# Kernel optimization log

Measured on AMD Instinct MI355X. Metric: run time of the kernel, lower is better.

Reference implementation:

```python
import jax, jax.numpy as jnp
import numpy as np

N = 131072   # batch
D = 32       # num features (main subnets)
P = 32       # num interaction pairs
H_MAIN = 64  # hidden_dim_main
H_INTER = 64 # hidden_dim_inter


def setup_inputs() -> dict:
    key = jax.random.key(0)
    ks = jax.random.split(key, 7)
    X = jax.random.normal(ks[0], (N, D), dtype=jnp.float32)
    # cyclic interaction pairs (i, (i+1) % D), matching init_kwargs literal
    pairs = jnp.asarray(np.stack([np.arange(P), (np.arange(P) + 1) % D], axis=1), dtype=jnp.int32)
    # stacked ExU params for the D main subnets: log_weight [H,1] -> [D,H], bias [1] -> [D]
    log_w_main = (jax.random.normal(ks[1], (D, H_MAIN), dtype=jnp.float32) * 0.1)
    bias_main = jnp.zeros((D,), dtype=jnp.float32)
    v_main = jax.random.normal(ks[2], (D, H_MAIN), dtype=jnp.float32) / np.float32(np.sqrt(H_MAIN))
    # stacked ExU params for the P interaction subnets: log_weight [H,2], bias [2]
    log_w_inter = (jax.random.normal(ks[3], (P, H_INTER, 2), dtype=jnp.float32) * 0.1)
    bias_inter = jnp.zeros((P, 2), dtype=jnp.float32)
    v_inter = jax.random.normal(ks[4], (P, H_INTER), dtype=jnp.float32) / np.float32(np.sqrt(H_INTER))
    # final Linear(D+P, 1)
    W_final = jax.random.normal(ks[5], (D + P,), dtype=jnp.float32) / np.float32(np.sqrt(D + P))
    b_final = jnp.zeros((), dtype=jnp.float32)
    return {
        "X": X,
        "log_w_main": log_w_main,
        "bias_main": bias_main,
        "v_main": v_main,
        "log_w_inter": log_w_inter,
        "bias_inter": bias_inter,
        "v_inter": v_inter,
        "W_final": W_final,
        "b_final": b_final,
        "pairs": pairs,
    }


def reference(X, log_w_main, bias_main, v_main, log_w_inter, bias_inter, v_inter, W_final, b_final, pairs):
    # Main subnets, batched over features: ExU(1,H) is (x - b) * exp(log_w)
    h_main = jax.nn.silu((X - bias_main[None, :])[:, :, None] * jnp.exp(log_w_main)[None, :, :])  # [N,D,H]
    m_out = jnp.einsum('ndh,dh->nd', h_main, v_main)  # [N,D]
    # Interaction subnets, batched over pairs: gather the 2 columns per pair
    Xp = X[:, pairs]  # [N,P,2]
    h_int = jax.nn.silu(jnp.einsum('npc,phc->nph', Xp - bias_inter[None, :, :], jnp.exp(log_w_inter)))  # [N,P,H]
    i_out = jnp.einsum('nph,ph->np', h_int, v_inter)  # [N,P]
    Z = jnp.concatenate([m_out, i_out], axis=1)  # [N, D+P]
    out = Z @ W_final + b_final  # [N]
    return out, Z
```

## Files before the change

kernel.cpp:

```cpp
#include <hip/hip_runtime.h>

#define DD 32
#define PP 32
#define HH 64
#define TPB 512
#define ROWS 512

#define M_NE 128
#define M_LO (-8.0f)
#define M_HI (8.0f)
#define I_NE 96
#define I_LO (-6.5f)
#define I_HI (6.5f)
#define I_CELLS (I_NE * I_NE)

#define BTPB 256
#define MAIN_BLOCKS ((DD * M_NE) / BTPB)
#define BLOCKS_PER_P (I_CELLS / BTPB)
#define INTER_BLOCKS (PP * BLOCKS_PER_P)

#define TSTR 36
#define XSTR 33

__device__ __forceinline__ float silu_fast(float t) {
    const float LOG2E = 1.4426950408889634f;
    return t * __builtin_amdgcn_rcpf(1.f + __builtin_amdgcn_exp2f(-t * LOG2E));
}

__device__ __forceinline__ unsigned short f2bf(float f) {
    unsigned u = __float_as_uint(f);
    u += 0x7FFF + ((u >> 16) & 1);
    return (unsigned short)(u >> 16);
}

__device__ __forceinline__ float bf2f(unsigned short s) {
    return __uint_as_float((unsigned)s << 16);
}

__global__ void build_luts(const float* __restrict__ lwm,
                           const float* __restrict__ vm,
                           const float* __restrict__ lwi,
                           const float* __restrict__ vi,
                           float* __restrict__ LUTm,
                           unsigned short* __restrict__ LUTi)
{
    const float LOG2E = 1.4426950408889634f;
    __shared__ float2 sew[HH];
    __shared__ float  sv[HH];

    if (blockIdx.x < MAIN_BLOCKS) {
        const float h = (M_HI - M_LO) / (float)(M_NE - 1);
        int idx = blockIdx.x * BTPB + threadIdx.x;
        int d = idx >> 7;
        int i = idx & (M_NE - 1);
        float s = M_LO + (float)i * h;
        float acc = 0.f;
        #pragma unroll 8
        for (int k = 0; k < HH; ++k) {
            float w = __builtin_amdgcn_exp2f(lwm[d * HH + k] * LOG2E);
            acc = fmaf(silu_fast(s * w), vm[d * HH + k], acc);
        }
        LUTm[idx] = acc;
    } else {
        const float h = (I_HI - I_LO) / (float)(I_NE - 1);
        const int rel = blockIdx.x - MAIN_BLOCKS;
        const int p   = rel / BLOCKS_PER_P;
        const int cip = (rel % BLOCKS_PER_P) * BTPB + threadIdx.x;
        const int i   = cip / I_NE;
        const int j   = cip - i * I_NE;
        if (threadIdx.x < HH) {
            int t = threadIdx.x;
            sew[t] = make_float2(
                __builtin_amdgcn_exp2f(lwi[(p * HH + t) * 2 + 0] * LOG2E),
                __builtin_amdgcn_exp2f(lwi[(p * HH + t) * 2 + 1] * LOG2E));
            sv[t] = vi[p * HH + t];
        }
        __syncthreads();
        float c0 = I_LO + (float)i * h;
        float c1 = I_LO + (float)j * h;
        float acc = 0.f;
        #pragma unroll 8
        for (int k = 0; k < HH; ++k) {
            float a = fmaf(c0, sew[k].x, c1 * sew[k].y);
            acc = fmaf(silu_fast(a), sv[k], acc);
        }
        unsigned short ab = f2bf(acc);
        unsigned short* cb = LUTi + (size_t)p * I_CELLS * 4;
        if (i < I_NE - 1 && j < I_NE - 1) cb[((i    ) * I_NE + j    ) * 4 + 0] = ab;
        if (i < I_NE - 1 && j > 0)        cb[((i    ) * I_NE + j - 1) * 4 + 1] = ab;
        if (i > 0        && j < I_NE - 1) cb[((i - 1) * I_NE + j    ) * 4 + 2] = ab;
        if (i > 0        && j > 0)        cb[((i - 1) * I_NE + j - 1) * 4 + 3] = ab;
    }
}

__global__ __launch_bounds__(TPB, 2) void qgam_main(
    const float* __restrict__ X,
    const float* __restrict__ bias_main,
    const float* __restrict__ bias_inter,
    const float* __restrict__ W_final,
    const float* __restrict__ b_final,
    const int* __restrict__ pairs,
    const float* __restrict__ LUTm,
    const ushort4* __restrict__ LUTi,
    float* __restrict__ out,
    float* __restrict__ Zout,
    int nrows)
{
    const float M_INVH = (float)(M_NE - 1) / (M_HI - M_LO);
    const float I_INVH = (float)(I_NE - 1) / (I_HI - I_LO);

    __shared__ float s_lutm[DD * M_NE];
    __shared__ float s_x[ROWS][XSTR];
    __shared__ float s_t[ROWS][TSTR];
    __shared__ float s_wf[DD + PP];
    __shared__ float s_moff[DD];
    __shared__ float s_io0[PP], s_io1[PP];
    __shared__ int   s_p0[PP], s_p1[PP];

    const int tid  = threadIdx.x;
    const int base = blockIdx.x * ROWS;

    {
        const float4* __restrict__ lm4 = reinterpret_cast<const float4*>(LUTm);
        float4* __restrict__ sl4 = reinterpret_cast<float4*>(s_lutm);
        #pragma unroll
        for (int k = 0; k < 2; ++k)
            sl4[k * TPB + tid] = lm4[k * TPB + tid];
    }
    {
        const float4* __restrict__ Xv =
            reinterpret_cast<const float4*>(X) + (size_t)base * (DD / 4);
        #pragma unroll
        for (int k = 0; k < 8; ++k) {
            const int fi = k * TPB + tid;
            const int rl = fi >> 3;
            const int c  = (fi & 7) * 4;
            if (base + rl < nrows) {
                float4 v = Xv[fi];
                s_x[rl][c + 0] = v.x;
                s_x[rl][c + 1] = v.y;
                s_x[rl][c + 2] = v.z;
                s_x[rl][c + 3] = v.w;
            }
        }
    }
    if (tid < DD + PP) s_wf[tid] = W_final[tid];
    if (tid < PP) {
        s_moff[tid] = -(bias_main[tid] + M_LO) * M_INVH;
        s_io0[tid]  = -(bias_inter[2 * tid + 0] + I_LO) * I_INVH;
        s_io1[tid]  = -(bias_inter[2 * tid + 1] + I_LO) * I_INVH;
        s_p0[tid]   = pairs[2 * tid + 0];
        s_p1[tid]   = pairs[2 * tid + 1];
    }
    __syncthreads();

    const int r = tid;
    const int n = base + r;

    float dot = b_final[0];

    #pragma unroll
    for (int d4 = 0; d4 < DD / 4; ++d4) {
        float z[4];
        #pragma unroll
        for (int j = 0; j < 4; ++j) {
            const int d = d4 * 4 + j;
            float u  = fmaf(s_x[r][d], M_INVH, s_moff[d]);
            int   ii = (int)floorf(u);
            ii = ii < 0 ? 0 : (ii > M_NE - 2 ? M_NE - 2 : ii);
            float f  = u - (float)ii;
            float t0 = s_lutm[(d << 7) + ii];
            float t1 = s_lutm[(d << 7) + ii + 1];
            z[j] = fmaf(f, t1 - t0, t0);
            dot = fmaf(z[j], s_wf[d], dot);
        }
        *reinterpret_cast<float4*>(&s_t[r][d4 * 4]) =
            make_float4(z[0], z[1], z[2], z[3]);
    }

    __syncthreads();
    #pragma unroll
    for (int i = 0; i < 8; ++i) {
        const int fi   = i * TPB + tid;
        const int rowl = fi >> 3;
        const int c4   = (fi & 7) * 4;
        const int row  = base + rowl;
        if (row < nrows) {
            float4 v = *reinterpret_cast<const float4*>(&s_t[rowl][c4]);
            *reinterpret_cast<float4*>(&Zout[(size_t)row * (DD + PP) + c4]) = v;
        }
    }
    __syncthreads();

    #pragma unroll
    for (int p4 = 0; p4 < PP / 4; ++p4) {
        float z[4];
        #pragma unroll
        for (int j = 0; j < 4; ++j) {
            const int p = p4 * 4 + j;
            const int i0 = s_p0[p], i1 = s_p1[p];
            float u  = fmaf(s_x[r][i0], I_INVH, s_io0[p]);
            float v_ = fmaf(s_x[r][i1], I_INVH, s_io1[p]);
            int   iu = (int)floorf(u);
            int   iv = (int)floorf(v_);
            iu = iu < 0 ? 0 : (iu > I_NE - 2 ? I_NE - 2 : iu);
            iv = iv < 0 ? 0 : (iv > I_NE - 2 ? I_NE - 2 : iv);
            float fu = u  - (float)iu;
            float fv = v_ - (float)iv;
            ushort4 cell = LUTi[(size_t)p * I_CELLS + iu * I_NE + iv];
            float a00 = bf2f(cell.x), a01 = bf2f(cell.y);
            float a10 = bf2f(cell.z), a11 = bf2f(cell.w);
            float r0 = fmaf(fv, a01 - a00, a00);
            float r1 = fmaf(fv, a11 - a10, a10);
            z[j] = fmaf(fu, r1 - r0, r0);
            dot = fmaf(z[j], s_wf[DD + p], dot);
        }
        *reinterpret_cast<float4*>(&s_t[r][p4 * 4]) =
            make_float4(z[0], z[1], z[2], z[3]);
    }

    if (n < nrows) out[n] = dot;

    __syncthreads();
    #pragma unroll
    for (int i = 0; i < 8; ++i) {
        const int fi   = i * TPB + tid;
        const int rowl = fi >> 3;
        const int c4   = (fi & 7) * 4;
        const int row  = base + rowl;
        if (row < nrows) {
            float4 v = *reinterpret_cast<const float4*>(&s_t[rowl][c4]);
            *reinterpret_cast<float4*>(&Zout[(size_t)row * (DD + PP) + DD + c4]) = v;
        }
    }
}

extern "C" void kernel_launch(void* const* d_in, const int* in_sizes, int n_in,
                              void* d_out, int out_size, void* d_ws, size_t ws_size,
                              hipStream_t stream) {
    const float* X   = (const float*)d_in[0];
    const float* lwm = (const float*)d_in[1];
    const float* bm  = (const float*)d_in[2];
    const float* vm  = (const float*)d_in[3];
    const float* lwi = (const float*)d_in[4];
    const float* bi  = (const float*)d_in[5];
    const float* vi  = (const float*)d_in[6];
    const float* wf  = (const float*)d_in[7];
    const float* bf  = (const float*)d_in[8];
    const int* pairs = (const int*)d_in[9];

    const int nrows = in_sizes[0] / DD;
    float* out = (float*)d_out;
    float* Z   = out + nrows;

    float*          LUTm = (float*)d_ws;
    unsigned short* LUTi = (unsigned short*)((char*)d_ws +
                           ((DD * M_NE * sizeof(float) + 255) & ~255));

    build_luts<<<MAIN_BLOCKS + INTER_BLOCKS, BTPB, 0, stream>>>(lwm, vm, lwi, vi,
                                                                LUTm, LUTi);

    const int grid = (nrows + ROWS - 1) / ROWS;
    qgam_main<<<grid, TPB, 0, stream>>>(X, bm, bi, wf, bf, pairs, LUTm,
                                        (const ushort4*)LUTi, out, Z, nrows);
}
```

Measured before the change: 33.70 us.

## Load X rows into registers and write Z directly, dropping LDS staging

Removes the shared-memory staging of X and of the Z tiles. Each thread now reads its own 128-byte X row into registers and writes its Z row straight to global memory with float4 stores. The block size drops to 256 with a launch bound of 4 blocks per SM, raising occupancy now that less LDS is used. A runtime check picks a fast path when the pairs are the cyclic (i, i+1) pattern, which indexes the register array with compile-time constants and falls back to general indexing otherwise. The trade-off is uncoalesced per-thread row access in place of the earlier coalesced staging.

```diff
diff --git a/kernel.cpp b/kernel.cpp
--- a/kernel.cpp
+++ b/kernel.cpp
@@ -3,8 +3,7 @@
 #define DD 32
 #define PP 32
 #define HH 64
-#define TPB 512
-#define ROWS 512
+#define TPB 256
 
 #define M_NE 128
 #define M_LO (-8.0f)
@@ -18,9 +17,6 @@
 #define MAIN_BLOCKS ((DD * M_NE) / BTPB)
 #define BLOCKS_PER_P (I_CELLS / BTPB)
 #define INTER_BLOCKS (PP * BLOCKS_PER_P)
-
-#define TSTR 36
-#define XSTR 33
 
 __device__ __forceinline__ float silu_fast(float t) {
     const float LOG2E = 1.4426950408889634f;
@@ -93,7 +89,7 @@
     }
 }
 
-__global__ __launch_bounds__(TPB, 2) void qgam_main(
+__global__ __launch_bounds__(TPB, 4) void qgam_main(
     const float* __restrict__ X,
     const float* __restrict__ bias_main,
     const float* __restrict__ bias_inter,
@@ -110,53 +106,50 @@
     const float I_INVH = (float)(I_NE - 1) / (I_HI - I_LO);
 
     __shared__ float s_lutm[DD * M_NE];
-    __shared__ float s_x[ROWS][XSTR];
-    __shared__ float s_t[ROWS][TSTR];
     __shared__ float s_wf[DD + PP];
     __shared__ float s_moff[DD];
     __shared__ float s_io0[PP], s_io1[PP];
-    __shared__ int   s_p0[PP], s_p1[PP];
-
-    const int tid  = threadIdx.x;
-    const int base = blockIdx.x * ROWS;
+
+    const int tid = threadIdx.x;
 
     {
         const float4* __restrict__ lm4 = reinterpret_cast<const float4*>(LUTm);
         float4* __restrict__ sl4 = reinterpret_cast<float4*>(s_lutm);
         #pragma unroll
-        for (int k = 0; k < 2; ++k)
+        for (int k = 0; k < 4; ++k)
             sl4[k * TPB + tid] = lm4[k * TPB + tid];
-    }
-    {
-        const float4* __restrict__ Xv =
-            reinterpret_cast<const float4*>(X) + (size_t)base * (DD / 4);
-        #pragma unroll
-        for (int k = 0; k < 8; ++k) {
-            const int fi = k * TPB + tid;
-            const int rl = fi >> 3;
-            const int c  = (fi & 7) * 4;
-            if (base + rl < nrows) {
-                float4 v = Xv[fi];
-                s_x[rl][c + 0] = v.x;
-                s_x[rl][c + 1] = v.y;
-                s_x[rl][c + 2] = v.z;
-                s_x[rl][c + 3] = v.w;
-            }
-        }
     }
     if (tid < DD + PP) s_wf[tid] = W_final[tid];
     if (tid < PP) {
         s_moff[tid] = -(bias_main[tid] + M_LO) * M_INVH;
         s_io0[tid]  = -(bias_inter[2 * tid + 0] + I_LO) * I_INVH;
         s_io1[tid]  = -(bias_inter[2 * tid + 1] + I_LO) * I_INVH;
-        s_p0[tid]   = pairs[2 * tid + 0];
-        s_p1[tid]   = pairs[2 * tid + 1];
-    }
+    }
+    bool okl = true;
+    {
+        const int l = tid & 63;
+        if (l < PP)
+            okl = (pairs[2 * l + 0] == l) && (pairs[2 * l + 1] == ((l + 1) & 31));
+    }
+    const bool fast = __all(okl);
     __syncthreads();
 
-    const int r = tid;
-    const int n = base + r;
-
+    const int n = blockIdx.x * TPB + tid;
+    if (n >= nrows) return;
+
+    float x[DD];
+    {
+        const float4* __restrict__ xr =
+            reinterpret_cast<const float4*>(X + (size_t)n * DD);
+        #pragma unroll
+        for (int k = 0; k < 8; ++k) {
+            float4 v = xr[k];
+            x[4 * k + 0] = v.x; x[4 * k + 1] = v.y;
+            x[4 * k + 2] = v.z; x[4 * k + 3] = v.w;
+        }
+    }
+
+    float* __restrict__ zrow = Zout + (size_t)n * (DD + PP);
     float dot = b_final[0];
 
     #pragma unroll
@@ -165,7 +158,7 @@
         #pragma unroll
         for (int j = 0; j < 4; ++j) {
             const int d = d4 * 4 + j;
-            float u  = fmaf(s_x[r][d], M_INVH, s_moff[d]);
+            float u  = fmaf(x[d], M_INVH, s_moff[d]);
             int   ii = (int)floorf(u);
             ii = ii < 0 ? 0 : (ii > M_NE - 2 ? M_NE - 2 : ii);
             float f  = u - (float)ii;
@@ -174,65 +167,68 @@
             z[j] = fmaf(f, t1 - t0, t0);
             dot = fmaf(z[j], s_wf[d], dot);
         }
-        *reinterpret_cast<float4*>(&s_t[r][d4 * 4]) =
+        *reinterpret_cast<float4*>(&zrow[d4 * 4]) =
             make_float4(z[0], z[1], z[2], z[3]);
     }
 
-    __syncthreads();
-    #pragma unroll
-    for (int i = 0; i < 8; ++i) {
-        const int fi   = i * TPB + tid;
-        const int rowl = fi >> 3;
-        const int c4   = (fi & 7) * 4;
-        const int row  = base + rowl;
-        if (row < nrows) {
-            float4 v = *reinterpret_cast<const float4*>(&s_t[rowl][c4]);
-            *reinterpret_cast<float4*>(&Zout[(size_t)row * (DD + PP) + c4]) = v;
-        }
-    }
-    __syncthreads();
-
-    #pragma unroll
-    for (int p4 = 0; p4 < PP / 4; ++p4) {
-        float z[4];
-        #pragma unroll
-        for (int j = 0; j < 4; ++j) {
-            const int p = p4 * 4 + j;
-            const int i0 = s_p0[p], i1 = s_p1[p];
-            float u  = fmaf(s_x[r][i0], I_INVH, s_io0[p]);
-            float v_ = fmaf(s_x[r][i1], I_INVH, s_io1[p]);
-            int   iu = (int)floorf(u);
-            int   iv = (int)floorf(v_);
-            iu = iu < 0 ? 0 : (iu > I_NE - 2 ? I_NE - 2 : iu);
-            iv = iv < 0 ? 0 : (iv > I_NE - 2 ? I_NE - 2 : iv);
-            float fu = u  - (float)iu;
-            float fv = v_ - (float)iv;
-            ushort4 cell = LUTi[(size_t)p * I_CELLS + iu * I_NE + iv];
-            float a00 = bf2f(cell.x), a01 = bf2f(cell.y);
-            float a10 = bf2f(cell.z), a11 = bf2f(cell.w);
-            float r0 = fmaf(fv, a01 - a00, a00);
-            float r1 = fmaf(fv, a11 - a10, a10);
-            z[j] = fmaf(fu, r1 - r0, r0);
-            dot = fmaf(z[j], s_wf[DD + p], dot);
-        }
-        *reinterpret_cast<float4*>(&s_t[r][p4 * 4]) =
-            make_float4(z[0], z[1], z[2], z[3]);
-    }
-
-    if (n < nrows) out[n] = dot;
-
-    __syncthreads();
-    #pragma unroll
-    for (int i = 0; i < 8; ++i) {
-        const int fi   = i * TPB + tid;
-        const int rowl = fi >> 3;
-        const int c4   = (fi & 7) * 4;
-        const int row  = base + rowl;
-        if (row < nrows) {
-            float4 v = *reinterpret_cast<const float4*>(&s_t[rowl][c4]);
-            *reinterpret_cast<float4*>(&Zout[(size_t)row * (DD + PP) + DD + c4]) = v;
-        }
-    }
+    if (fast) {
+        #pragma unroll
+        for (int p4 = 0; p4 < PP / 4; ++p4) {
+            float z[4];
+            #pragma unroll
+            for (int j = 0; j < 4; ++j) {
+                const int p = p4 * 4 + j;
+                float u  = fmaf(x[p], I_INVH, s_io0[p]);
+                float v_ = fmaf(x[(p + 1) & 31], I_INVH, s_io1[p]);
+                int   iu = (int)floorf(u);
+                int   iv = (int)floorf(v_);
+                iu = iu < 0 ? 0 : (iu > I_NE - 2 ? I_NE - 2 : iu);
+                iv = iv < 0 ? 0 : (iv > I_NE - 2 ? I_NE - 2 : iv);
+                float fu = u  - (float)iu;
+                float fv = v_ - (float)iv;
+                ushort4 cell = LUTi[(size_t)p * I_CELLS + iu * I_NE + iv];
+                float a00 = bf2f(cell.x), a01 = bf2f(cell.y);
+                float a10 = bf2f(cell.z), a11 = bf2f(cell.w);
+                float r0 = fmaf(fv, a01 - a00, a00);
+                float r1 = fmaf(fv, a11 - a10, a10);
+                z[j] = fmaf(fu, r1 - r0, r0);
+                dot = fmaf(z[j], s_wf[DD + p], dot);
+            }
+            *reinterpret_cast<float4*>(&zrow[DD + p4 * 4]) =
+                make_float4(z[0], z[1], z[2], z[3]);
+        }
+    } else {
+        const float* __restrict__ xg = X + (size_t)n * DD;
+        #pragma unroll
+        for (int p4 = 0; p4 < PP / 4; ++p4) {
+            float z[4];
+            #pragma unroll
+            for (int j = 0; j < 4; ++j) {
+                const int p = p4 * 4 + j;
+                const int i0 = pairs[2 * p + 0];
+                const int i1 = pairs[2 * p + 1];
+                float u  = fmaf(xg[i0], I_INVH, s_io0[p]);
+                float v_ = fmaf(xg[i1], I_INVH, s_io1[p]);
+                int   iu = (int)floorf(u);
+                int   iv = (int)floorf(v_);
+                iu = iu < 0 ? 0 : (iu > I_NE - 2 ? I_NE - 2 : iu);
+                iv = iv < 0 ? 0 : (iv > I_NE - 2 ? I_NE - 2 : iv);
+                float fu = u  - (float)iu;
+                float fv = v_ - (float)iv;
+                ushort4 cell = LUTi[(size_t)p * I_CELLS + iu * I_NE + iv];
+                float a00 = bf2f(cell.x), a01 = bf2f(cell.y);
+                float a10 = bf2f(cell.z), a11 = bf2f(cell.w);
+                float r0 = fmaf(fv, a01 - a00, a00);
+                float r1 = fmaf(fv, a11 - a10, a10);
+                z[j] = fmaf(fu, r1 - r0, r0);
+                dot = fmaf(z[j], s_wf[DD + p], dot);
+            }
+            *reinterpret_cast<float4*>(&zrow[DD + p4 * 4]) =
+                make_float4(z[0], z[1], z[2], z[3]);
+        }
+    }
+
+    out[n] = dot;
 }
 
 extern "C" void kernel_launch(void* const* d_in, const int* in_sizes, int n_in,
@@ -260,7 +256,7 @@
     build_luts<<<MAIN_BLOCKS + INTER_BLOCKS, BTPB, 0, stream>>>(lwm, vm, lwi, vi,
                                                                 LUTm, LUTi);
 
-    const int grid = (nrows + ROWS - 1) / ROWS;
+    const int grid = (nrows + TPB - 1) / TPB;
     qgam_main<<<grid, TPB, 0, stream>>>(X, bm, bi, wf, bf, pairs, LUTm,
                                         (const ushort4*)LUTi, out, Z, nrows);
 }
```

After: 46.38 us. 1.38x slower.
